# Performance work log

Measured on AMD Instinct MI355X. Metric: run time of the kernel, lower is better.

## Reference

```python
import jax, jax.numpy as jnp
import numpy as np

B, S, D = 8, 2048, 512

def setup_inputs() -> dict:
    key = jax.random.key(0)
    ks = jax.random.split(key, 9)
    scale = 1.0 / np.sqrt(D)
    q = jax.random.normal(ks[0], (B, S, D), dtype=jnp.float32)
    k = jax.random.normal(ks[1], (B, S, D), dtype=jnp.float32)
    v = jax.random.normal(ks[2], (B, S, D), dtype=jnp.float32)
    # causal mask, broadcast over batch: True = attend
    mask = jnp.tril(jnp.ones((S, S), dtype=bool))[None, :, :]
    Wq = jax.random.normal(ks[3], (D, D), dtype=jnp.float32) * scale
    bq = jax.random.normal(ks[4], (D,), dtype=jnp.float32) * scale
    Wk = jax.random.normal(ks[5], (D, D), dtype=jnp.float32) * scale
    bk = jax.random.normal(ks[6], (D,), dtype=jnp.float32) * scale
    Wv = jax.random.normal(ks[7], (D, D), dtype=jnp.float32) * scale
    bv = jax.random.normal(ks[8], (D,), dtype=jnp.float32) * scale
    return {"q": q, "k": k, "v": v, "mask": mask,
            "Wq": Wq, "bq": bq, "Wk": Wk, "bk": bk, "Wv": Wv, "bv": bv}

def reference(q, k, v, mask, Wq, bq, Wk, bk, Wv, bv):
    # torch nn.Linear: x @ W^T + b
    Q = jnp.einsum('bsd,ed->bse', q, Wq) + bq
    K = jnp.einsum('bsd,ed->bse', k, Wk) + bk
    V = jnp.einsum('bsd,ed->bse', v, Wv) + bv
    scores = jnp.einsum('bqd,bkd->bqk', Q, K) / jnp.sqrt(jnp.float32(D))
    scores = jnp.where(mask, scores, jnp.float32(-1e9))
    prob = jax.nn.softmax(scores, axis=-1)
    out = jnp.einsum('bqk,bkd->bqd', prob, V)
    return out
```

## Files before the change

kernel.cpp:

```cpp
#include <hip/hip_runtime.h>
#include <stdint.h>
#include <stddef.h>
#include <math.h>

typedef _Float16 half8 __attribute__((ext_vector_type(8)));
typedef float f32x4 __attribute__((ext_vector_type(4)));

#define SCALE_QK 0.04419417382415922f

__device__ __forceinline__ void gload16(const void* g, void* lds) {
  __builtin_amdgcn_global_load_lds(
      (const __attribute__((address_space(1))) void*)g,
      (__attribute__((address_space(3))) void*)lds,
      16, 0, 0);
}

__device__ __forceinline__ void run_kloop(const _Float16* A, const _Float16* B,
                                          int lda, int ldb, int kIters,
                                          _Float16* As, _Float16* Bs,
                                          f32x4 (&acc)[4][4])
{
  const int tid  = threadIdx.x;
  const int lane = tid & 63;
  const int w    = tid >> 6;
  const int wm   = w >> 1, wn = w & 1;
  const int srow = tid >> 3;
  const int sg   = tid & 7;
  const int swz  = sg ^ (srow & 7);
  const int fr   = lane & 15;
  const int fq   = lane >> 4;
  const int fx   = lane & 7;

  auto stage = [&](int it) {
    const int k0 = it * 64;
    #pragma unroll
    for (int i = 0; i < 4; ++i) {
      gload16(A + (size_t)(i*32 + srow) * lda + (k0 + swz*8), As + i*2048 + w*512);
      gload16(B + (size_t)(i*32 + srow) * ldb + (k0 + swz*8), Bs + i*2048 + w*512);
    }
  };
  auto compute = [&]() {
    #pragma unroll
    for (int ks = 0; ks < 2; ++ks) {
      half8 av[4], bv[4];
      const int slot = (ks*4 + fq) ^ fx;
      #pragma unroll
      for (int i = 0; i < 4; ++i) {
        av[i] = *(const half8*)(As + (wm*64 + i*16 + fr)*64 + slot*8);
        bv[i] = *(const half8*)(Bs + (wn*64 + i*16 + fr)*64 + slot*8);
      }
      #pragma unroll
      for (int i = 0; i < 4; ++i) {
        #pragma unroll
        for (int j = 0; j < 4; ++j)
          acc[i][j] = __builtin_amdgcn_mfma_f32_16x16x32_f16(av[i], bv[j], acc[i][j], 0, 0, 0);
      }
    }
  };

  stage(0);
  __syncthreads();
  for (int it = 0; ; ) {
    compute();
    if (++it >= kIters) break;
    __syncthreads();
    stage(it);
    __syncthreads();
  }
}

__global__ __launch_bounds__(256) void k_cvtw(const float* __restrict__ Wq,
                                              const float* __restrict__ Wk,
                                              const float* __restrict__ Wv,
                                              _Float16* __restrict__ Wb)
{
  const int t = blockIdx.x * 256 + threadIdx.x;
  const int base = t * 8;
  const int z = base >> 18;
  const int off = base & 262143;
  const float* src = (z == 0) ? Wq : ((z == 1) ? Wk : Wv);
  f32x4 a = *(const f32x4*)(src + off);
  f32x4 b = *(const f32x4*)(src + off + 4);
  half8 h;
  h[0]=(_Float16)a[0]; h[1]=(_Float16)a[1]; h[2]=(_Float16)a[2]; h[3]=(_Float16)a[3];
  h[4]=(_Float16)b[0]; h[5]=(_Float16)b[1]; h[6]=(_Float16)b[2]; h[7]=(_Float16)b[3];
  *(half8*)(Wb + base) = h;
}

__global__ __launch_bounds__(256) void k_cvtin(const float* __restrict__ q,
                                               const float* __restrict__ k,
                                               const float* __restrict__ v,
                                               _Float16* __restrict__ X)
{
  const size_t t = (size_t)blockIdx.x * 256 + threadIdx.x;
  const size_t base = t * 8;
  const int z = (int)(base >> 23);
  const size_t off = base & 8388607;
  const float* src = (z == 0) ? q : ((z == 1) ? k : v);
  f32x4 a = *(const f32x4*)(src + off);
  f32x4 b = *(const f32x4*)(src + off + 4);
  half8 h;
  h[0]=(_Float16)a[0]; h[1]=(_Float16)a[1]; h[2]=(_Float16)a[2]; h[3]=(_Float16)a[3];
  h[4]=(_Float16)b[0]; h[5]=(_Float16)b[1]; h[6]=(_Float16)b[2]; h[7]=(_Float16)b[3];
  *(half8*)(X + base) = h;
}

__global__ __launch_bounds__(256) void k_proj(const _Float16* __restrict__ X,
                                              const _Float16* __restrict__ Wb,
                                              const float* __restrict__ bq,
                                              const float* __restrict__ bk,
                                              const float* __restrict__ bv,
                                              _Float16* __restrict__ Qb,
                                              _Float16* __restrict__ Kb,
                                              _Float16* __restrict__ Vb)
{
  __shared__ __align__(16) _Float16 As[128*64];
  __shared__ __align__(16) _Float16 Bs[128*64];
  const int bid = blockIdx.x;
  const int xcd = bid & 7, i = bid >> 3;
  const int p = xcd * 48 + (i >> 2);
  const int nt = i & 3;
  const int z = p >> 7, mt = p & 127;

  const _Float16* A  = X + (size_t)z * 8388608;
  const float* bia   = (z == 0) ? bq : (z == 1) ? bk : bv;
  const _Float16* B  = Wb + (size_t)z * 512 * 512;
  _Float16* C        = (z == 0) ? Qb : (z == 1) ? Kb : Vb;

  f32x4 acc[4][4] = {};
  run_kloop(A + (size_t)mt*128*512, B + (size_t)nt*128*512, 512, 512, 8, As, Bs, acc);

  const int lane = threadIdx.x & 63, w = threadIdx.x >> 6;
  const int wm = w >> 1, wn = w & 1;
  const int fr = lane & 15, fq = lane >> 4;
  #pragma unroll
  for (int j = 0; j < 4; ++j) {
    const int col = nt*128 + wn*64 + j*16 + fr;
    const float bval = bia[col];
    #pragma unroll
    for (int i2 = 0; i2 < 4; ++i2) {
      const int row = mt*128 + wm*64 + i2*16 + fq*4;
      #pragma unroll
      for (int r = 0; r < 4; ++r)
        C[(size_t)(row + r) * 512 + col] = (_Float16)(acc[i2][j][r] + bval);
    }
  }
}

__global__ __launch_bounds__(256) void k_trans(const _Float16* __restrict__ Vb,
                                               _Float16* __restrict__ Vt)
{
  __shared__ __align__(16) _Float16 t[64][72];
  const int st = blockIdx.x, dt = blockIdx.y, b = blockIdx.z;
  const int r = threadIdx.x >> 2, g = threadIdx.x & 3;
  const _Float16* src = Vb + ((size_t)b*2048 + st*64 + r)*512 + dt*64 + g*16;
  half8 v0 = *(const half8*)src;
  half8 v1 = *(const half8*)(src + 8);
  *(half8*)&t[r][g*16]     = v0;
  *(half8*)&t[r][g*16 + 8] = v1;
  __syncthreads();
  half8 o0, o1;
  #pragma unroll
  for (int i2 = 0; i2 < 8; ++i2) o0[i2] = t[g*16 + i2][r];
  #pragma unroll
  for (int i2 = 0; i2 < 8; ++i2) o1[i2] = t[g*16 + 8 + i2][r];
  _Float16* dst = Vt + ((size_t)b*512 + dt*64 + r)*2048 + st*64 + g*16;
  *(half8*)dst       = o0;
  *(half8*)(dst + 8) = o1;
}

__global__ __launch_bounds__(256) void k_scores(const _Float16* __restrict__ Qb,
                                                const _Float16* __restrict__ Kb,
                                                _Float16* __restrict__ P)
{
  const int bid = blockIdx.x;
  const int b = bid & 7;
  const int t = bid >> 3;
  int qt = (int)((sqrtf(8.0f * (float)t + 1.0f) - 1.0f) * 0.5f);
  int base = (qt * (qt + 1)) >> 1;
  if (t < base)                { --qt; base = (qt * (qt + 1)) >> 1; }
  else if (t >= base + qt + 1) { ++qt; base = (qt * (qt + 1)) >> 1; }
  const int kt = t - base;

  __shared__ __align__(16) _Float16 As[128*64];
  __shared__ __align__(16) _Float16 Bs[128*64];
  f32x4 acc[4][4] = {};
  run_kloop(Qb + ((size_t)b*2048 + qt*128)*512,
            Kb + ((size_t)b*2048 + kt*128)*512,
            512, 512, 8, As, Bs, acc);
  const int lane = threadIdx.x & 63, w = threadIdx.x >> 6;
  const int wm = w >> 1, wn = w & 1;
  const int fr = lane & 15, fq = lane >> 4;
  #pragma unroll
  for (int i = 0; i < 4; ++i) {
    const int row = qt*128 + wm*64 + i*16 + fq*4;
    #pragma unroll
    for (int j = 0; j < 4; ++j) {
      const int col = kt*128 + wn*64 + j*16 + fr;
      #pragma unroll
      for (int r = 0; r < 4; ++r)
        P[((size_t)b*2048 + row + r) * 2048 + col] = (_Float16)(acc[i][j][r] * SCALE_QK);
    }
  }
}

__global__ __launch_bounds__(256) void k_softmax(_Float16* __restrict__ P)
{
  const int lane = threadIdx.x & 63;
  const int row  = blockIdx.x * 4 + (threadIdx.x >> 6);
  const int qIdx = row & 2047;
  _Float16* p = P + (size_t)row * 2048;
  const int L    = qIdx + 1;
  const int Lpad = ((qIdx >> 7) + 1) * 128;

  float m = -1e30f, s = 0.f;
  for (int i0 = lane * 8; i0 < L; i0 += 512) {
    float xv[8];
    if (i0 + 8 <= L) {
      half8 x = *(const half8*)(p + i0);
      #pragma unroll
      for (int j = 0; j < 8; ++j) xv[j] = (float)x[j];
    } else {
      #pragma unroll
      for (int j = 0; j < 8; ++j) xv[j] = (i0 + j < L) ? (float)p[i0 + j] : -1e30f;
    }
    float cm = xv[0];
    #pragma unroll
    for (int j = 1; j < 8; ++j) cm = fmaxf(cm, xv[j]);
    const float mn = fmaxf(m, cm);
    float cs = 0.f;
    #pragma unroll
    for (int j = 0; j < 8; ++j) cs += __expf(xv[j] - mn);
    s = s * __expf(m - mn) + cs;
    m = mn;
  }
  #pragma unroll
  for (int d = 1; d < 64; d <<= 1) {
    const float mo = __shfl_xor(m, d, 64);
    const float so = __shfl_xor(s, d, 64);
    const float mn = fmaxf(m, mo);
    s = s * __expf(m - mn) + so * __expf(mo - mn);
    m = mn;
  }
  const float inv = 1.0f / s;

  for (int i0 = lane * 8; i0 < Lpad; i0 += 512) {
    half8 o;
    if (i0 + 8 <= L) {
      half8 x = *(const half8*)(p + i0);
      #pragma unroll
      for (int j = 0; j < 8; ++j) o[j] = (_Float16)(__expf((float)x[j] - m) * inv);
    } else {
      #pragma unroll
      for (int j = 0; j < 8; ++j) {
        const int idx = i0 + j;
        o[j] = (idx < L) ? (_Float16)(__expf((float)p[idx] - m) * inv) : (_Float16)0.f;
      }
    }
    *(half8*)(p + i0) = o;
  }
}

__global__ __launch_bounds__(256) void k_pv(const _Float16* __restrict__ P,
                                            const _Float16* __restrict__ Vt,
                                            float* __restrict__ Out)
{
  const int bid = blockIdx.x;
  const int b = bid & 7;
  const int r0 = bid >> 3;
  const int qi = r0 >> 2, dt = r0 & 3;
  const int qt = (qi & 1) ? (15 - (qi >> 1)) : (qi >> 1);

  __shared__ __align__(16) _Float16 As[128*64];
  __shared__ __align__(16) _Float16 Bs[128*64];
  f32x4 acc[4][4] = {};
  run_kloop(P  + ((size_t)b*2048 + qt*128)*2048,
            Vt + ((size_t)b*512  + dt*128)*2048,
            2048, 2048, (qt + 1) * 2, As, Bs, acc);
  const int lane = threadIdx.x & 63, w = threadIdx.x >> 6;
  const int wm = w >> 1, wn = w & 1;
  const int fr = lane & 15, fq = lane >> 4;
  #pragma unroll
  for (int i = 0; i < 4; ++i) {
    const int row = qt*128 + wm*64 + i*16 + fq*4;
    #pragma unroll
    for (int j = 0; j < 4; ++j) {
      const int col = dt*128 + wn*64 + j*16 + fr;
      #pragma unroll
      for (int r = 0; r < 4; ++r)
        Out[((size_t)b*2048 + row + r) * 512 + col] = acc[i][j][r];
    }
  }
}

extern "C" void kernel_launch(void* const* d_in, const int* in_sizes, int n_in,
                              void* d_out, int out_size, void* d_ws, size_t ws_size,
                              hipStream_t stream) {
  (void)in_sizes; (void)n_in; (void)out_size;
  const float* q  = (const float*)d_in[0];
  const float* k  = (const float*)d_in[1];
  const float* v  = (const float*)d_in[2];
  const float* Wq = (const float*)d_in[4];
  const float* bq = (const float*)d_in[5];
  const float* Wk = (const float*)d_in[6];
  const float* bk = (const float*)d_in[7];
  const float* Wv = (const float*)d_in[8];
  const float* bv = (const float*)d_in[9];

  const size_t OFF_P  = 0;
  const size_t OFF_Q  = (size_t)64 << 20;
  const size_t OFF_K  = (size_t)80 << 20;
  const size_t OFF_V  = (size_t)96 << 20;
  const size_t OFF_VT = (size_t)112 << 20;
  const size_t OFF_W  = (size_t)128 << 20;
  const size_t NEEDED = OFF_W + (size_t)3 * 512 * 512 * sizeof(_Float16);
  if (ws_size < NEEDED) return;

  char* ws = (char*)d_ws;
  _Float16* P  = (_Float16*)(ws + OFF_P);
  _Float16* X  = (_Float16*)(ws + OFF_P);
  _Float16* Qb = (_Float16*)(ws + OFF_Q);
  _Float16* Kb = (_Float16*)(ws + OFF_K);
  _Float16* Vb = (_Float16*)(ws + OFF_V);
  _Float16* Vt = (_Float16*)(ws + OFF_VT);
  _Float16* Wb = (_Float16*)(ws + OFF_W);
  float* Out = (float*)d_out;

  k_cvtw   <<<dim3(384),      dim3(256), 0, stream>>>(Wq, Wk, Wv, Wb);
  k_cvtin  <<<dim3(12288),    dim3(256), 0, stream>>>(q, k, v, X);
  k_proj   <<<dim3(1536),     dim3(256), 0, stream>>>(X, Wb, bq, bk, bv, Qb, Kb, Vb);
  k_trans  <<<dim3(32, 8, 8), dim3(256), 0, stream>>>(Vb, Vt);
  k_scores <<<dim3(1088),     dim3(256), 0, stream>>>(Qb, Kb, P);
  k_softmax<<<dim3(4096),     dim3(256), 0, stream>>>(P);
  k_pv     <<<dim3(512),      dim3(256), 0, stream>>>(P, Vt, Out);
}
```

Measured before the change: 283.2 us.

## Fuse input conversion and V transpose into projection, stage epilogues via LDS

The projection kernel now loads fp32 q/k/v directly into shared memory and converts them to fp16 when reading MFMA operands, which removes the separate conversion kernel and its fp16 intermediate round trip. The V projection also writes the transposed Vt from its LDS-staged output tile, so the transpose kernel goes away. The projection and score epilogues stage results in LDS and write coalesced 16-byte rows instead of scattered 2-byte stores. The cost is twice the A-tile traffic into LDS, extra shared memory per block (possibly lower occupancy), and conversion work repeated across the four N tiles.

After: 286.1 us. Within noise of the previous version (+1.0%).

```diff
diff --git a/kernel.cpp b/kernel.cpp
--- a/kernel.cpp
+++ b/kernel.cpp
@@ -15,9 +15,10 @@
       16, 0, 0);
 }
 
-__device__ __forceinline__ void run_kloop(const _Float16* A, const _Float16* B,
+template<bool A_F32>
+__device__ __forceinline__ void run_kloop(const void* Aptr, const _Float16* B,
                                           int lda, int ldb, int kIters,
-                                          _Float16* As, _Float16* Bs,
+                                          void* AsRaw, _Float16* Bs,
                                           f32x4 (&acc)[4][4])
 {
   const int tid  = threadIdx.x;
@@ -33,21 +34,51 @@
 
   auto stage = [&](int it) {
     const int k0 = it * 64;
-    #pragma unroll
-    for (int i = 0; i < 4; ++i) {
-      gload16(A + (size_t)(i*32 + srow) * lda + (k0 + swz*8), As + i*2048 + w*512);
+    if constexpr (A_F32) {
+      const float* A = (const float*)Aptr;
+      float* As32 = (float*)AsRaw;
+      #pragma unroll
+      for (int i = 0; i < 8; ++i) {
+        const int n = i * 4 + w;
+        const int row = n * 4 + (lane >> 4);
+        const int g = (lane & 15) ^ ((row & 7) << 1);
+        gload16(A + (size_t)row * lda + k0 + g * 4, As32 + n * 256);
+      }
+    } else {
+      const _Float16* A = (const _Float16*)Aptr;
+      _Float16* As16 = (_Float16*)AsRaw;
+      #pragma unroll
+      for (int i = 0; i < 4; ++i)
+        gload16(A + (size_t)(i*32 + srow) * lda + (k0 + swz*8), As16 + i*2048 + w*512);
+    }
+    #pragma unroll
+    for (int i = 0; i < 4; ++i)
       gload16(B + (size_t)(i*32 + srow) * ldb + (k0 + swz*8), Bs + i*2048 + w*512);
-    }
   };
+
   auto compute = [&]() {
     #pragma unroll
     for (int ks = 0; ks < 2; ++ks) {
       half8 av[4], bv[4];
-      const int slot = (ks*4 + fq) ^ fx;
       #pragma unroll
       for (int i = 0; i < 4; ++i) {
-        av[i] = *(const half8*)(As + (wm*64 + i*16 + fr)*64 + slot*8);
-        bv[i] = *(const half8*)(Bs + (wn*64 + i*16 + fr)*64 + slot*8);
+        const int r = wm*64 + i*16 + fr;
+        if constexpr (A_F32) {
+          const float* As32 = (const float*)AsRaw;
+          const int m = ks*4 + fq;
+          const int g0 = (2*m) ^ ((r & 7) << 1);
+          const float* pa = As32 + r*64 + g0*4;
+          f32x4 a0 = *(const f32x4*)pa;
+          f32x4 a1 = *(const f32x4*)(pa + 4);
+          half8 h;
+          h[0]=(_Float16)a0[0]; h[1]=(_Float16)a0[1]; h[2]=(_Float16)a0[2]; h[3]=(_Float16)a0[3];
+          h[4]=(_Float16)a1[0]; h[5]=(_Float16)a1[1]; h[6]=(_Float16)a1[2]; h[7]=(_Float16)a1[3];
+          av[i] = h;
+        } else {
+          const _Float16* As16 = (const _Float16*)AsRaw;
+          av[i] = *(const half8*)(As16 + r*64 + (((ks*4+fq) ^ fx))*8);
+        }
+        bv[i] = *(const half8*)(Bs + (wn*64 + i*16 + fr)*64 + (((ks*4+fq) ^ fx))*8);
       }
       #pragma unroll
       for (int i = 0; i < 4; ++i) {
@@ -87,92 +118,86 @@
   *(half8*)(Wb + base) = h;
 }
 
-__global__ __launch_bounds__(256) void k_cvtin(const float* __restrict__ q,
-                                               const float* __restrict__ k,
-                                               const float* __restrict__ v,
-                                               _Float16* __restrict__ X)
-{
-  const size_t t = (size_t)blockIdx.x * 256 + threadIdx.x;
-  const size_t base = t * 8;
-  const int z = (int)(base >> 23);
-  const size_t off = base & 8388607;
-  const float* src = (z == 0) ? q : ((z == 1) ? k : v);
-  f32x4 a = *(const f32x4*)(src + off);
-  f32x4 b = *(const f32x4*)(src + off + 4);
-  half8 h;
-  h[0]=(_Float16)a[0]; h[1]=(_Float16)a[1]; h[2]=(_Float16)a[2]; h[3]=(_Float16)a[3];
-  h[4]=(_Float16)b[0]; h[5]=(_Float16)b[1]; h[6]=(_Float16)b[2]; h[7]=(_Float16)b[3];
-  *(half8*)(X + base) = h;
-}
-
-__global__ __launch_bounds__(256) void k_proj(const _Float16* __restrict__ X,
+__global__ __launch_bounds__(256) void k_proj(const float* __restrict__ q,
+                                              const float* __restrict__ k,
+                                              const float* __restrict__ v,
                                               const _Float16* __restrict__ Wb,
                                               const float* __restrict__ bq,
                                               const float* __restrict__ bk,
                                               const float* __restrict__ bv,
                                               _Float16* __restrict__ Qb,
                                               _Float16* __restrict__ Kb,
-                                              _Float16* __restrict__ Vb)
-{
-  __shared__ __align__(16) _Float16 As[128*64];
-  __shared__ __align__(16) _Float16 Bs[128*64];
+                                              _Float16* __restrict__ Vb,
+                                              _Float16* __restrict__ Vt)
+{
+  __shared__ __align__(16) _Float16 sh[24576];
+  float*    As32 = (float*)sh;
+  _Float16* Bs   = sh + 16384;
+  _Float16* Cs   = sh;
+
   const int bid = blockIdx.x;
-  const int xcd = bid & 7, i = bid >> 3;
-  const int p = xcd * 48 + (i >> 2);
-  const int nt = i & 3;
+  const int xcd = bid & 7, ii = bid >> 3;
+  const int p = xcd * 48 + (ii >> 2);
+  const int nt = ii & 3;
   const int z = p >> 7, mt = p & 127;
 
-  const _Float16* A  = X + (size_t)z * 8388608;
-  const float* bia   = (z == 0) ? bq : (z == 1) ? bk : bv;
-  const _Float16* B  = Wb + (size_t)z * 512 * 512;
-  _Float16* C        = (z == 0) ? Qb : (z == 1) ? Kb : Vb;
+  const float* A   = (z == 0) ? q  : (z == 1) ? k  : v;
+  const float* bia = (z == 0) ? bq : (z == 1) ? bk : bv;
+  const _Float16* B = Wb + (size_t)z * 512 * 512;
+  _Float16* C      = (z == 0) ? Qb : (z == 1) ? Kb : Vb;
 
   f32x4 acc[4][4] = {};
-  run_kloop(A + (size_t)mt*128*512, B + (size_t)nt*128*512, 512, 512, 8, As, Bs, acc);
-
-  const int lane = threadIdx.x & 63, w = threadIdx.x >> 6;
+  run_kloop<true>(A + (size_t)mt*128*512, B + (size_t)nt*128*512, 512, 512, 8, As32, Bs, acc);
+
+  const int tid = threadIdx.x;
+  const int lane = tid & 63, w = tid >> 6;
   const int wm = w >> 1, wn = w & 1;
   const int fr = lane & 15, fq = lane >> 4;
+  const int row0 = mt * 128, col0 = nt * 128;
+
+  __syncthreads();
   #pragma unroll
   for (int j = 0; j < 4; ++j) {
-    const int col = nt*128 + wn*64 + j*16 + fr;
-    const float bval = bia[col];
-    #pragma unroll
-    for (int i2 = 0; i2 < 4; ++i2) {
-      const int row = mt*128 + wm*64 + i2*16 + fq*4;
+    const float bval = bia[col0 + wn*64 + j*16 + fr];
+    #pragma unroll
+    for (int i = 0; i < 4; ++i) {
       #pragma unroll
       for (int r = 0; r < 4; ++r)
-        C[(size_t)(row + r) * 512 + col] = (_Float16)(acc[i2][j][r] + bval);
-    }
-  }
-}
-
-__global__ __launch_bounds__(256) void k_trans(const _Float16* __restrict__ Vb,
-                                               _Float16* __restrict__ Vt)
-{
-  __shared__ __align__(16) _Float16 t[64][72];
-  const int st = blockIdx.x, dt = blockIdx.y, b = blockIdx.z;
-  const int r = threadIdx.x >> 2, g = threadIdx.x & 3;
-  const _Float16* src = Vb + ((size_t)b*2048 + st*64 + r)*512 + dt*64 + g*16;
-  half8 v0 = *(const half8*)src;
-  half8 v1 = *(const half8*)(src + 8);
-  *(half8*)&t[r][g*16]     = v0;
-  *(half8*)&t[r][g*16 + 8] = v1;
-  __syncthreads();
-  half8 o0, o1;
-  #pragma unroll
-  for (int i2 = 0; i2 < 8; ++i2) o0[i2] = t[g*16 + i2][r];
-  #pragma unroll
-  for (int i2 = 0; i2 < 8; ++i2) o1[i2] = t[g*16 + 8 + i2][r];
-  _Float16* dst = Vt + ((size_t)b*512 + dt*64 + r)*2048 + st*64 + g*16;
-  *(half8*)dst       = o0;
-  *(half8*)(dst + 8) = o1;
+        Cs[(wm*64 + i*16 + fq*4 + r) * 128 + wn*64 + j*16 + fr] =
+            (_Float16)(acc[i][j][r] + bval);
+    }
+  }
+  __syncthreads();
+
+  const int rr = tid >> 4, cc = tid & 15;
+  #pragma unroll
+  for (int m2 = 0; m2 < 8; ++m2) {
+    const int r = m2*16 + rr;
+    half8 val = *(const half8*)(Cs + r*128 + cc*8);
+    *(half8*)(C + (size_t)(row0 + r)*512 + col0 + cc*8) = val;
+  }
+  if (z == 2) {
+    const int b = row0 >> 11, s0 = row0 & 2047;
+    #pragma unroll
+    for (int m2 = 0; m2 < 8; ++m2) {
+      const int d = m2*16 + rr;
+      half8 vv;
+      #pragma unroll
+      for (int x = 0; x < 8; ++x) vv[x] = Cs[(cc*8 + x)*128 + d];
+      *(half8*)(Vt + ((size_t)b*512 + col0 + d)*2048 + s0 + cc*8) = vv;
+    }
+  }
 }
 
 __global__ __launch_bounds__(256) void k_scores(const _Float16* __restrict__ Qb,
                                                 const _Float16* __restrict__ Kb,
                                                 _Float16* __restrict__ P)
 {
+  __shared__ __align__(16) _Float16 sh[16384];
+  _Float16* As = sh;
+  _Float16* Bs = sh + 8192;
+  _Float16* Cs = sh;
+
   const int bid = blockIdx.x;
   const int b = bid & 7;
   const int t = bid >> 3;
@@ -182,25 +207,35 @@
   else if (t >= base + qt + 1) { ++qt; base = (qt * (qt + 1)) >> 1; }
   const int kt = t - base;
 
-  __shared__ __align__(16) _Float16 As[128*64];
-  __shared__ __align__(16) _Float16 Bs[128*64];
   f32x4 acc[4][4] = {};
-  run_kloop(Qb + ((size_t)b*2048 + qt*128)*512,
-            Kb + ((size_t)b*2048 + kt*128)*512,
-            512, 512, 8, As, Bs, acc);
-  const int lane = threadIdx.x & 63, w = threadIdx.x >> 6;
+  run_kloop<false>(Qb + ((size_t)b*2048 + qt*128)*512,
+                   Kb + ((size_t)b*2048 + kt*128)*512,
+                   512, 512, 8, As, Bs, acc);
+
+  const int tid = threadIdx.x;
+  const int lane = tid & 63, w = tid >> 6;
   const int wm = w >> 1, wn = w & 1;
   const int fr = lane & 15, fq = lane >> 4;
+
+  __syncthreads();
   #pragma unroll
   for (int i = 0; i < 4; ++i) {
-    const int row = qt*128 + wm*64 + i*16 + fq*4;
     #pragma unroll
     for (int j = 0; j < 4; ++j) {
-      const int col = kt*128 + wn*64 + j*16 + fr;
       #pragma unroll
       for (int r = 0; r < 4; ++r)
-        P[((size_t)b*2048 + row + r) * 2048 + col] = (_Float16)(acc[i][j][r] * SCALE_QK);
-    }
+        Cs[(wm*64 + i*16 + fq*4 + r) * 128 + wn*64 + j*16 + fr] =
+            (_Float16)(acc[i][j][r] * SCALE_QK);
+    }
+  }
+  __syncthreads();
+
+  const int rr = tid >> 4, cc = tid & 15;
+  #pragma unroll
+  for (int m2 = 0; m2 < 8; ++m2) {
+    const int r = m2*16 + rr;
+    half8 val = *(const half8*)(Cs + r*128 + cc*8);
+    *(half8*)(P + ((size_t)b*2048 + qt*128 + r)*2048 + kt*128 + cc*8) = val;
   }
 }
 
@@ -265,18 +300,18 @@
                                             const _Float16* __restrict__ Vt,
                                             float* __restrict__ Out)
 {
+  __shared__ __align__(16) _Float16 As[8192];
+  __shared__ __align__(16) _Float16 Bs[8192];
   const int bid = blockIdx.x;
   const int b = bid & 7;
   const int r0 = bid >> 3;
   const int qi = r0 >> 2, dt = r0 & 3;
   const int qt = (qi & 1) ? (15 - (qi >> 1)) : (qi >> 1);
 
-  __shared__ __align__(16) _Float16 As[128*64];
-  __shared__ __align__(16) _Float16 Bs[128*64];
   f32x4 acc[4][4] = {};
-  run_kloop(P  + ((size_t)b*2048 + qt*128)*2048,
-            Vt + ((size_t)b*512  + dt*128)*2048,
-            2048, 2048, (qt + 1) * 2, As, Bs, acc);
+  run_kloop<false>(P  + ((size_t)b*2048 + qt*128)*2048,
+                   Vt + ((size_t)b*512  + dt*128)*2048,
+                   2048, 2048, (qt + 1) * 2, As, Bs, acc);
   const int lane = threadIdx.x & 63, w = threadIdx.x >> 6;
   const int wm = w >> 1, wn = w & 1;
   const int fr = lane & 15, fq = lane >> 4;
@@ -318,7 +353,6 @@
 
   char* ws = (char*)d_ws;
   _Float16* P  = (_Float16*)(ws + OFF_P);
-  _Float16* X  = (_Float16*)(ws + OFF_P);
   _Float16* Qb = (_Float16*)(ws + OFF_Q);
   _Float16* Kb = (_Float16*)(ws + OFF_K);
   _Float16* Vb = (_Float16*)(ws + OFF_V);
@@ -326,11 +360,9 @@
   _Float16* Wb = (_Float16*)(ws + OFF_W);
   float* Out = (float*)d_out;
 
-  k_cvtw   <<<dim3(384),      dim3(256), 0, stream>>>(Wq, Wk, Wv, Wb);
-  k_cvtin  <<<dim3(12288),    dim3(256), 0, stream>>>(q, k, v, X);
-  k_proj   <<<dim3(1536),     dim3(256), 0, stream>>>(X, Wb, bq, bk, bv, Qb, Kb, Vb);
-  k_trans  <<<dim3(32, 8, 8), dim3(256), 0, stream>>>(Vb, Vt);
-  k_scores <<<dim3(1088),     dim3(256), 0, stream>>>(Qb, Kb, P);
-  k_softmax<<<dim3(4096),     dim3(256), 0, stream>>>(P);
-  k_pv     <<<dim3(512),      dim3(256), 0, stream>>>(P, Vt, Out);
-}
+  k_cvtw   <<<dim3(384),  dim3(256), 0, stream>>>(Wq, Wk, Wv, Wb);
+  k_proj   <<<dim3(1536), dim3(256), 0, stream>>>(q, k, v, Wb, bq, bk, bv, Qb, Kb, Vb, Vt);
+  k_scores <<<dim3(1088), dim3(256), 0, stream>>>(Qb, Kb, P);
+  k_softmax<<<dim3(4096), dim3(256), 0, stream>>>(P);
+  k_pv     <<<dim3(512),  dim3(256), 0, stream>>>(P, Vt, Out);
+}
```
